# Kernel tuning notes

Measured on AMD Instinct MI355X. Metric: run time of the kernel, lower is better.

## Reference

```python
import jax, jax.numpy as jnp
import numpy as np

E, D, H, F = 3, 512, 8, 2048
B, V, L = 32, 21, 128
DH = D // H
EPS = 1e-5


def setup_inputs() -> dict:
    key = jax.random.key(0)
    ks = jax.random.split(key, 8)
    s = 0.02
    def p(k, shape):
        return (jax.random.normal(k, shape, jnp.float32) * s)
    return {
        "x": jax.random.normal(ks[0], (B, V, L, D), jnp.float32),
        "Wq": p(ks[1], (E, D, D)), "bq": jnp.zeros((E, D), jnp.float32),
        "Wk": p(ks[2], (E, D, D)), "bk": jnp.zeros((E, D), jnp.float32),
        "Wv": p(ks[3], (E, D, D)), "bv": jnp.zeros((E, D), jnp.float32),
        "Wo": p(ks[4], (E, D, D)), "bo": jnp.zeros((E, D), jnp.float32),
        "W1": p(ks[5], (E, D, F)), "b1": jnp.zeros((E, F), jnp.float32),
        "W2": p(ks[6], (E, F, D)), "b2": jnp.zeros((E, D), jnp.float32),
        "g1": jnp.ones((E, D), jnp.float32), "be1": jnp.zeros((E, D), jnp.float32),
        "g2": jnp.ones((E, D), jnp.float32), "be2": jnp.zeros((E, D), jnp.float32),
    }


def _batchnorm(x, gamma, beta):
    # x: [N, L, D]; BatchNorm1d(d_model) on x.transpose(-2,-1) == per-D-channel
    # stats over (N, L) axes (train-mode, biased variance).
    mean = jnp.mean(x, axis=(0, 1))
    var = jnp.var(x, axis=(0, 1))
    return (x - mean) * jax.lax.rsqrt(var + EPS) * gamma + beta


def _layer(x, prev_scores, Wq, bq, Wk, bk, Wv, bv, Wo, bo,
           W1, b1, W2, b2, g1, be1, g2, be2):
    N = x.shape[0]
    # multi-head projections -> [N, H, L, DH]
    q = (x @ Wq + bq).reshape(N, L, H, DH).transpose(0, 2, 1, 3)
    k = (x @ Wk + bk).reshape(N, L, H, DH).transpose(0, 2, 1, 3)
    v = (x @ Wv + bv).reshape(N, L, H, DH).transpose(0, 2, 1, 3)
    scores = jnp.einsum('nhld,nhmd->nhlm', q, k) / jnp.sqrt(jnp.float32(DH))
    if prev_scores is not None:
        scores = scores + prev_scores  # RealFormer-style residual score add
    attn = jax.nn.softmax(scores, axis=-1)
    ctx = jnp.einsum('nhlm,nhmd->nhld', attn, v)
    ctx = ctx.transpose(0, 2, 1, 3).reshape(N, L, D)
    x_ = ctx @ Wo + bo
    x = _batchnorm(x + x_, g1, be1)
    ffn = jax.nn.gelu(x @ W1 + b1, approximate=False) @ W2 + b2
    x = _batchnorm(x + ffn, g2, be2)
    return x, scores


def reference(x, Wq, bq, Wk, bk, Wv, bv, Wo, bo, W1, b1, W2, b2,
              g1, be1, g2, be2):
    h = x.reshape(-1, L, D)  # (B*V, L, D)
    scores = None
    for i in range(E):
        h, scores = _layer(h, scores,
                           Wq[i], bq[i], Wk[i], bk[i], Wv[i], bv[i],
                           Wo[i], bo[i], W1[i], b1[i], W2[i], b2[i],
                           g1[i], be1[i], g2[i], be2[i])
    return h
```

## Files before the change

kernel.cpp:

```cpp
#include <hip/hip_runtime.h>
#include <hip/hip_bf16.h>


typedef unsigned short u16;
typedef unsigned int u32;
typedef __attribute__((ext_vector_type(8))) short short8;
typedef __attribute__((ext_vector_type(4))) float floatx4;
typedef __attribute__((ext_vector_type(4))) unsigned short ushort4v;

#define DEV static __device__ __forceinline__

DEV u16 f2bf(float f) {
    union { float f; u32 u; } a; a.f = f;
    u32 r = a.u + 0x7FFF + ((a.u >> 16) & 1);
    return (u16)(r >> 16);
}
DEV float bf2f(u16 b) {
    union { u32 u; float f; } a; a.u = ((u32)b) << 16; return a.f;
}

DEV void gload16(const void* g, void* l) {
    __builtin_amdgcn_global_load_lds((const __attribute__((address_space(1))) void*)g,
                                     (__attribute__((address_space(3))) void*)l, 16, 0, 0);
}

__global__ void wtrans(const float* __restrict__ W, u16* __restrict__ out, int K, int N) {
    __shared__ float tile[32][33];
    const int k0 = blockIdx.x * 32, n0 = blockIdx.y * 32;
    const int tx = threadIdx.x & 31, ty = threadIdx.x >> 5;
#pragma unroll
    for (int j = 0; j < 4; ++j) {
        int r = ty + j * 8;
        tile[r][tx] = W[(size_t)(k0 + r) * N + n0 + tx];
    }
    __syncthreads();
#pragma unroll
    for (int j = 0; j < 4; ++j) {
        int r = ty + j * 8;
        out[(size_t)(n0 + r) * K + k0 + tx] = f2bf(tile[tx][r]);
    }
}

__global__ void bias_concat(const float* __restrict__ bq, const float* __restrict__ bk,
                            const float* __restrict__ bv, float* __restrict__ bqkv) {
    int t = blockIdx.x * 256 + threadIdx.x;
    if (t >= 3 * 1536) return;
    int e = t / 1536, c = t % 1536;
    float v = (c < 512) ? bq[e * 512 + c] : (c < 1024) ? bk[e * 512 + c - 512] : bv[e * 512 + c - 1024];
    bqkv[t] = v;
}

__global__ void xconvert(const float* __restrict__ x, u16* __restrict__ hb) {
    size_t i = ((size_t)blockIdx.x * 256 + threadIdx.x) * 8;
    float4 v0 = *(const float4*)&x[i];
    float4 v1 = *(const float4*)&x[i + 4];
    short8 o;
    o[0] = (short)f2bf(v0.x); o[1] = (short)f2bf(v0.y); o[2] = (short)f2bf(v0.z); o[3] = (short)f2bf(v0.w);
    o[4] = (short)f2bf(v1.x); o[5] = (short)f2bf(v1.y); o[6] = (short)f2bf(v1.z); o[7] = (short)f2bf(v1.w);
    *(short8*)&hb[i] = o;
}

template <int EPI>
__global__ __launch_bounds__(512)
void gemm_bt(const u16* __restrict__ A, int lda, const u16* __restrict__ Bt,
             const float* __restrict__ bias, const u16* __restrict__ res,
             u16* __restrict__ out, int N, int K, float* __restrict__ stats) {
    __shared__ u16 sA[2][4096];
    __shared__ u16 sB[2][4096];
    const int tid = threadIdx.x;
    const int wave = tid >> 6, lane = tid & 63;
    const int wm = wave >> 2, wn = wave & 3;
    const int m0 = blockIdx.y * 128, n0 = blockIdx.x * 128;
    const int fr = lane & 15, fq = lane >> 4;
    const int srow = lane >> 2, scol = (lane & 3) * 8;

    floatx4 acc[4][2] = {};
    const int NT = K >> 6;

    for (int kt = 0; kt < NT; ++kt) {
        __syncthreads();
        {
            const int ra = wave * 16 + srow;
            const size_t arow = (size_t)(m0 + ra) * lda + kt * 64 + scol;
            const size_t brow = (size_t)(n0 + ra) * (size_t)K + kt * 64 + scol;
#pragma unroll
            for (int kk = 0; kk < 2; ++kk) {
                gload16(A + arow + kk * 32, &sA[kk][wave * 512]);
                gload16(Bt + brow + kk * 32, &sB[kk][wave * 512]);
            }
        }
        __syncthreads();
#pragma unroll
        for (int kk = 0; kk < 2; ++kk) {
            short8 af[4], bfr[2];
#pragma unroll
            for (int m = 0; m < 4; ++m)
                af[m] = *(const short8*)&sA[kk][(wm * 64 + m * 16 + fr) * 32 + fq * 8];
#pragma unroll
            for (int nn = 0; nn < 2; ++nn)
                bfr[nn] = *(const short8*)&sB[kk][(wn * 32 + nn * 16 + fr) * 32 + fq * 8];
#pragma unroll
            for (int m = 0; m < 4; ++m)
#pragma unroll
                for (int nn = 0; nn < 2; ++nn)
                    acc[m][nn] = __builtin_amdgcn_mfma_f32_16x16x32_bf16(af[m], bfr[nn], acc[m][nn], 0, 0, 0);
        }
    }

    float ssum[2] = { 0.f, 0.f }, sqsum[2] = { 0.f, 0.f };
#pragma unroll
    for (int nn = 0; nn < 2; ++nn) {
        int col = n0 + wn * 32 + nn * 16 + fr;
        float bv = bias[col];
#pragma unroll
        for (int m = 0; m < 4; ++m) {
            int rowb = m0 + wm * 64 + m * 16 + fq * 4;
#pragma unroll
            for (int r = 0; r < 4; ++r) {
                size_t idx = (size_t)(rowb + r) * N + col;
                float v = acc[m][nn][r] + bv;
                if (EPI == 2) {
                    v += bf2f(res[idx]);
                    ssum[nn] += v;
                    sqsum[nn] += v * v;
                } else if (EPI == 1) {
                    v = 0.5f * v * (1.f + erff(v * 0.70710678118f));
                }
                out[idx] = f2bf(v);
            }
        }
    }
    if (EPI == 2) {
#pragma unroll
        for (int nn = 0; nn < 2; ++nn) {
            float s = ssum[nn], q = sqsum[nn];
            s += __shfl_xor(s, 16); s += __shfl_xor(s, 32);
            q += __shfl_xor(q, 16); q += __shfl_xor(q, 32);
            if (fq == 0) {
                int col = n0 + wn * 32 + nn * 16 + fr;
                atomicAdd(&stats[col], s);
                atomicAdd(&stats[512 + col], q);
            }
        }
    }
}

template <int HAS_PREV, int STORE_S>
__global__ __launch_bounds__(256)
void attn_kernel(u16* __restrict__ qkv, u16* __restrict__ scores) {
    const int bid = blockIdx.x;
    const int n = bid >> 3, h = bid & 7;
    const int tid = threadIdx.x, wave = tid >> 6, lane = tid & 63;
    const int wm = wave >> 1, wn = wave & 1;
    const int fr = lane & 15, fq = lane >> 4;

    __shared__ __align__(16) u16 uni[128 * 136];
    __shared__ __align__(16) u16 sV[64 * 136];
    __shared__ float sRed[128 * 2];

    u16 (*sQK)[128 * 32] = (u16(*)[128 * 32])uni;

    {
        const int t_ = wave;
        const int qk = t_ >> 1, kh = t_ & 1;
        const u16* base = qkv + (size_t)n * 128 * 1536 + qk * 512 + h * 64 + kh * 32 + (lane & 3) * 8;
        u16* dst = &sQK[t_][0];
        const int rr = lane >> 2;
#pragma unroll
        for (int c = 0; c < 8; ++c)
            gload16(base + (size_t)(c * 16 + rr) * 1536, dst + c * 512);
    }
    {
        const int mrow = tid >> 1;
        const int dh0 = (tid & 1) * 32;
        const u16* vsrc = qkv + (size_t)(n * 128 + mrow) * 1536 + 1024 + h * 64 + dh0;
#pragma unroll
        for (int j = 0; j < 4; ++j) {
            short8 vv = *(const short8*)&vsrc[j * 8];
#pragma unroll
            for (int e2 = 0; e2 < 8; ++e2)
                sV[(dh0 + j * 8 + e2) * 136 + mrow] = (u16)vv[e2];
        }
    }
    __syncthreads();

    floatx4 acc[4][4] = {};
#pragma unroll
    for (int kh = 0; kh < 2; ++kh) {
        short8 a[4], b[4];
#pragma unroll
        for (int m = 0; m < 4; ++m)
            a[m] = *(const short8*)&sQK[kh][(wm * 64 + m * 16 + fr) * 32 + fq * 8];
#pragma unroll
        for (int nn = 0; nn < 4; ++nn)
            b[nn] = *(const short8*)&sQK[2 + kh][(wn * 64 + nn * 16 + fr) * 32 + fq * 8];
#pragma unroll
        for (int m = 0; m < 4; ++m)
#pragma unroll
            for (int nn = 0; nn < 4; ++nn)
                acc[m][nn] = __builtin_amdgcn_mfma_f32_16x16x32_bf16(b[nn], a[m], acc[m][nn], 0, 0, 0);
    }

    const size_t tbase = ((size_t)bid * 256 + tid) * 64;
#pragma unroll
    for (int m = 0; m < 4; ++m) {
        short8 lo, hi;
        if (HAS_PREV) {
            lo = *(const short8*)&scores[tbase + m * 16];
            hi = *(const short8*)&scores[tbase + m * 16 + 8];
        }
#pragma unroll
        for (int nn = 0; nn < 4; ++nn)
#pragma unroll
            for (int r = 0; r < 4; ++r) {
                const int e = nn * 4 + r;
                float v = acc[m][nn][r] * 0.125f;
                if (HAS_PREV) v += bf2f((u16)(e < 8 ? lo[e] : hi[e - 8]));
                acc[m][nn][r] = v;
            }
        if (STORE_S) {
            short8 slo, shi;
#pragma unroll
            for (int nn = 0; nn < 4; ++nn)
#pragma unroll
                for (int r = 0; r < 4; ++r) {
                    const int e = nn * 4 + r;
                    u16 bv = f2bf(acc[m][nn][r]);
                    if (e < 8) slo[e] = (short)bv; else shi[e - 8] = (short)bv;
                }
            *(short8*)&scores[tbase + m * 16] = slo;
            *(short8*)&scores[tbase + m * 16 + 8] = shi;
        }
    }

#pragma unroll
    for (int m = 0; m < 4; ++m) {
        const int row = wm * 64 + m * 16 + fr;
        float mx = acc[m][0][0];
#pragma unroll
        for (int nn = 0; nn < 4; ++nn)
#pragma unroll
            for (int r = 0; r < 4; ++r) mx = fmaxf(mx, acc[m][nn][r]);
        mx = fmaxf(mx, __shfl_xor(mx, 16));
        mx = fmaxf(mx, __shfl_xor(mx, 32));
        if (fq == 0) sRed[row * 2 + wn] = mx;
    }
    __syncthreads();

    float rmax[4];
#pragma unroll
    for (int m = 0; m < 4; ++m) {
        const int row = wm * 64 + m * 16 + fr;
        rmax[m] = fmaxf(sRed[row * 2], sRed[row * 2 + 1]);
    }
    __syncthreads();

    u16* sP = uni;
#pragma unroll
    for (int m = 0; m < 4; ++m) {
        const int row = wm * 64 + m * 16 + fr;
        float sm = 0.f;
#pragma unroll
        for (int nn = 0; nn < 4; ++nn) {
#pragma unroll
            for (int r = 0; r < 4; ++r) {
                float p = __expf(acc[m][nn][r] - rmax[m]);
                acc[m][nn][r] = p;
                sm += p;
            }
        }
        sm += __shfl_xor(sm, 16);
        sm += __shfl_xor(sm, 32);
        if (fq == 0) sRed[row * 2 + wn] = sm;
#pragma unroll
        for (int nn = 0; nn < 4; ++nn) {
            ushort4v pv = { f2bf(acc[m][nn][0]), f2bf(acc[m][nn][1]),
                            f2bf(acc[m][nn][2]), f2bf(acc[m][nn][3]) };
            *(ushort4v*)&sP[row * 136 + wn * 64 + nn * 16 + fq * 4] = pv;
        }
    }
    __syncthreads();

    floatx4 acc2[4][2] = {};
#pragma unroll
    for (int k0 = 0; k0 < 128; k0 += 32) {
        short8 a[4], b[2];
#pragma unroll
        for (int m = 0; m < 4; ++m)
            a[m] = *(const short8*)&sP[(wm * 64 + m * 16 + fr) * 136 + k0 + fq * 8];
#pragma unroll
        for (int n2 = 0; n2 < 2; ++n2)
            b[n2] = *(const short8*)&sV[(wn * 32 + n2 * 16 + fr) * 136 + k0 + fq * 8];
#pragma unroll
        for (int m = 0; m < 4; ++m)
#pragma unroll
            for (int n2 = 0; n2 < 2; ++n2)
                acc2[m][n2] = __builtin_amdgcn_mfma_f32_16x16x32_bf16(b[n2], a[m], acc2[m][n2], 0, 0, 0);
    }

#pragma unroll
    for (int m = 0; m < 4; ++m) {
        const int row = wm * 64 + m * 16 + fr;
        const float inv = 1.f / (sRed[row * 2] + sRed[row * 2 + 1]);
#pragma unroll
        for (int n2 = 0; n2 < 2; ++n2) {
            const int dhb = wn * 32 + n2 * 16 + fq * 4;
            ushort4v o = { f2bf(acc2[m][n2][0] * inv), f2bf(acc2[m][n2][1] * inv),
                           f2bf(acc2[m][n2][2] * inv), f2bf(acc2[m][n2][3] * inv) };
            *(ushort4v*)&qkv[(size_t)(n * 128 + row) * 1536 + h * 64 + dhb] = o;
        }
    }
}

__global__ void zero_stats(float* s) { s[threadIdx.x] = 0.f; }

__global__ void bn_finalize(float* stats, int M) {
    int c = blockIdx.x * 256 + threadIdx.x;
    if (c >= 512) return;
    float mean = stats[c] / M;
    float var = stats[512 + c] / M - mean * mean;
    stats[c] = mean;
    stats[512 + c] = rsqrtf(var + 1e-5f);
}

template <int FINAL>
__global__ void bn_apply(const u16* __restrict__ y, const float* __restrict__ stats,
                         const float* __restrict__ gamma, const float* __restrict__ beta,
                         u16* __restrict__ outb, float* __restrict__ outf) {
    size_t i = ((size_t)blockIdx.x * 256 + threadIdx.x) * 8;
    short8 v = *(const short8*)&y[i];
    int c = (int)(i & 511);
    float o[8];
#pragma unroll
    for (int j = 0; j < 8; ++j) {
        float f = bf2f((u16)v[j]);
        o[j] = (f - stats[c + j]) * stats[512 + c + j] * gamma[c + j] + beta[c + j];
    }
    if (FINAL) {
        float4 a = { o[0], o[1], o[2], o[3] }, b = { o[4], o[5], o[6], o[7] };
        *(float4*)&outf[i] = a;
        *(float4*)&outf[i + 4] = b;
    } else {
        short8 ob;
#pragma unroll
        for (int j = 0; j < 8; ++j) ob[j] = (short)f2bf(o[j]);
        *(short8*)&outb[i] = ob;
    }
}

extern "C" void kernel_launch(void* const* d_in, const int* in_sizes, int n_in,
                              void* d_out, int out_size, void* d_ws, size_t ws_size,
                              hipStream_t stream) {
    const float* x  = (const float*)d_in[0];
    const float* Wq = (const float*)d_in[1];  const float* bq = (const float*)d_in[2];
    const float* Wk = (const float*)d_in[3];  const float* bk = (const float*)d_in[4];
    const float* Wv = (const float*)d_in[5];  const float* bv = (const float*)d_in[6];
    const float* Wo = (const float*)d_in[7];  const float* bo = (const float*)d_in[8];
    const float* W1 = (const float*)d_in[9];  const float* b1 = (const float*)d_in[10];
    const float* W2 = (const float*)d_in[11]; const float* b2 = (const float*)d_in[12];
    const float* g1 = (const float*)d_in[13]; const float* be1 = (const float*)d_in[14];
    const float* g2 = (const float*)d_in[15]; const float* be2 = (const float*)d_in[16];

    const int M = 86016;
    const int MC = 43008;

    char* ws = (char*)d_ws;
    size_t off = 0;
    auto alloc = [&](size_t bytes) -> void* {
        void* p = ws + off;
        off = (off + bytes + 255) & ~(size_t)255;
        return p;
    };
    u16* scores = (u16*)alloc((size_t)5376 * 16384 * 2);
    u16* hb     = (u16*)alloc((size_t)M * 512 * 2);
    u16* qkv    = (u16*)alloc((size_t)M * 1536 * 2);
    u16* Wqkvt  = (u16*)alloc((size_t)3 * 1536 * 512 * 2);
    u16* Wot    = (u16*)alloc((size_t)3 * 512 * 512 * 2);
    u16* W1t    = (u16*)alloc((size_t)3 * 2048 * 512 * 2);
    u16* W2t    = (u16*)alloc((size_t)3 * 512 * 2048 * 2);
    float* bqkv = (float*)alloc((size_t)3 * 1536 * 4);
    float* stats = (float*)alloc(1024 * 4);

    if (off > ws_size) return;

    for (int e = 0; e < 3; ++e) {
        wtrans<<<dim3(16, 16), 256, 0, stream>>>(Wq + (size_t)e * 512 * 512, Wqkvt + (size_t)e * 1536 * 512, 512, 512);
        wtrans<<<dim3(16, 16), 256, 0, stream>>>(Wk + (size_t)e * 512 * 512, Wqkvt + (size_t)e * 1536 * 512 + 512 * 512, 512, 512);
        wtrans<<<dim3(16, 16), 256, 0, stream>>>(Wv + (size_t)e * 512 * 512, Wqkvt + (size_t)e * 1536 * 512 + 1024 * 512, 512, 512);
        wtrans<<<dim3(16, 16), 256, 0, stream>>>(Wo + (size_t)e * 512 * 512, Wot + (size_t)e * 512 * 512, 512, 512);
        wtrans<<<dim3(16, 64), 256, 0, stream>>>(W1 + (size_t)e * 512 * 2048, W1t + (size_t)e * 2048 * 512, 512, 2048);
        wtrans<<<dim3(64, 16), 256, 0, stream>>>(W2 + (size_t)e * 2048 * 512, W2t + (size_t)e * 512 * 2048, 2048, 512);
    }
    bias_concat<<<18, 256, 0, stream>>>(bq, bk, bv, bqkv);
    xconvert<<<21504, 256, 0, stream>>>(x, hb);

    for (int e = 0; e < 3; ++e) {
        gemm_bt<0><<<dim3(12, 672), 512, 0, stream>>>(hb, 512, Wqkvt + (size_t)e * 1536 * 512,
                                                      bqkv + e * 1536, nullptr, qkv, 1536, 512, nullptr);
        if (e == 0)      attn_kernel<0, 1><<<5376, 256, 0, stream>>>(qkv, scores);
        else if (e == 1) attn_kernel<1, 1><<<5376, 256, 0, stream>>>(qkv, scores);
        else             attn_kernel<1, 0><<<5376, 256, 0, stream>>>(qkv, scores);
        zero_stats<<<1, 1024, 0, stream>>>(stats);
        gemm_bt<2><<<dim3(4, 672), 512, 0, stream>>>(qkv, 1536, Wot + (size_t)e * 512 * 512,
                                                     bo + e * 512, hb, hb, 512, 512, stats);
        bn_finalize<<<2, 256, 0, stream>>>(stats, M);
        bn_apply<0><<<21504, 256, 0, stream>>>(hb, stats, g1 + e * 512, be1 + e * 512, hb, nullptr);
        zero_stats<<<1, 1024, 0, stream>>>(stats);
        for (int c = 0; c < 2; ++c) {
            const u16* hc = hb + (size_t)c * MC * 512;
            gemm_bt<1><<<dim3(16, 336), 512, 0, stream>>>(hc, 512, W1t + (size_t)e * 2048 * 512,
                                                          b1 + e * 2048, nullptr, qkv, 2048, 512, nullptr);
            gemm_bt<2><<<dim3(4, 336), 512, 0, stream>>>(qkv, 2048, W2t + (size_t)e * 512 * 2048,
                                                         b2 + e * 512, hc, (u16*)hc, 512, 2048, stats);
        }
        bn_finalize<<<2, 256, 0, stream>>>(stats, M);
        if (e < 2)
            bn_apply<0><<<21504, 256, 0, stream>>>(hb, stats, g2 + e * 512, be2 + e * 512, hb, nullptr);
        else
            bn_apply<1><<<21504, 256, 0, stream>>>(hb, stats, g2 + e * 512, be2 + e * 512, nullptr, (float*)d_out);
    }
    (void)in_sizes; (void)n_in; (void)out_size;
}
```

Before: 3.273 ms.

## Fold BatchNorm affine into next-layer weights, biases and residual epilogue

Drops the separate BatchNorm apply passes over the activation buffer. The per-channel scale is folded into the transposed bf16 weights of the following GEMM (QKV or W1), and the shift is folded into its bias through a small matvec. The residual GEMM epilogue (new EPI 3) applies the same scale and shift to the un-normalized residual on the fly, so only the final output still needs an apply pass. Weight transposes are also batched over experts with a z grid dimension. Rescaling bf16 weights in place adds a second rounding step, and the normalized activation is never stored explicitly.

```diff
diff --git a/kernel.cpp b/kernel.cpp
--- a/kernel.cpp
+++ b/kernel.cpp
@@ -24,7 +24,10 @@
                                      (__attribute__((address_space(3))) void*)l, 16, 0, 0);
 }
 
-__global__ void wtrans(const float* __restrict__ W, u16* __restrict__ out, int K, int N) {
+__global__ void wtrans(const float* __restrict__ W, u16* __restrict__ out, int K, int N,
+                       int inStride, int outStride) {
+    W += (size_t)blockIdx.z * inStride;
+    out += (size_t)blockIdx.z * outStride;
     __shared__ float tile[32][33];
     const int k0 = blockIdx.x * 32, n0 = blockIdx.y * 32;
     const int tx = threadIdx.x & 31, ty = threadIdx.x >> 5;
@@ -60,11 +63,51 @@
     *(short8*)&hb[i] = o;
 }
 
+__global__ void zero_stats2(float* raw) { raw[blockIdx.x * 1024 + threadIdx.x] = 0.f; }
+
+__global__ void bn_finalize_st(const float* __restrict__ raw, const float* __restrict__ g,
+                               const float* __restrict__ be, float* __restrict__ fin, int M) {
+    int c = blockIdx.x * 256 + threadIdx.x;
+    if (c >= 512) return;
+    float mean = raw[c] / M;
+    float var = raw[512 + c] / M - mean * mean;
+    float s = rsqrtf(var + 1e-5f) * g[c];
+    fin[512 + c] = s;
+    fin[c] = be[c] - mean * s;
+}
+
+__global__ void bias_fold(const u16* __restrict__ Wt, const float* __restrict__ bias_in,
+                          const float* __restrict__ fin, float* __restrict__ bias_out) {
+    __shared__ float tsh[512];
+    for (int i = threadIdx.x; i < 512; i += 256) tsh[i] = fin[i];
+    __syncthreads();
+    int n = blockIdx.x * 256 + threadIdx.x;
+    const u16* w = Wt + (size_t)n * 512;
+    float acc = bias_in[n];
+    for (int k = 0; k < 512; k += 8) {
+        short8 wv = *(const short8*)&w[k];
+#pragma unroll
+        for (int j = 0; j < 8; ++j) acc += tsh[k + j] * bf2f((u16)wv[j]);
+    }
+    bias_out[n] = acc;
+}
+
+__global__ void weight_scale(u16* __restrict__ Wt, const float* __restrict__ fin) {
+    size_t i = ((size_t)blockIdx.x * 256 + threadIdx.x) * 8;
+    int k = (int)(i & 511);
+    short8 w = *(short8*)&Wt[i];
+    short8 o;
+#pragma unroll
+    for (int j = 0; j < 8; ++j) o[j] = (short)f2bf(bf2f((u16)w[j]) * fin[512 + k + j]);
+    *(short8*)&Wt[i] = o;
+}
+
 template <int EPI>
 __global__ __launch_bounds__(512)
 void gemm_bt(const u16* __restrict__ A, int lda, const u16* __restrict__ Bt,
              const float* __restrict__ bias, const u16* __restrict__ res,
-             u16* __restrict__ out, int N, int K, float* __restrict__ stats) {
+             u16* __restrict__ out, int N, int K, float* __restrict__ stats,
+             const float* __restrict__ finRes) {
     __shared__ u16 sA[2][4096];
     __shared__ u16 sB[2][4096];
     const int tid = threadIdx.x;
@@ -112,6 +155,8 @@
     for (int nn = 0; nn < 2; ++nn) {
         int col = n0 + wn * 32 + nn * 16 + fr;
         float bv = bias[col];
+        float rs = 0.f, rt = 0.f;
+        if (EPI == 3) { rs = finRes[512 + col]; rt = finRes[col]; }
 #pragma unroll
         for (int m = 0; m < 4; ++m) {
             int rowb = m0 + wm * 64 + m * 16 + fq * 4;
@@ -121,8 +166,10 @@
                 float v = acc[m][nn][r] + bv;
                 if (EPI == 2) {
                     v += bf2f(res[idx]);
-                    ssum[nn] += v;
-                    sqsum[nn] += v * v;
+                    ssum[nn] += v; sqsum[nn] += v * v;
+                } else if (EPI == 3) {
+                    v += rs * bf2f(res[idx]) + rt;
+                    ssum[nn] += v; sqsum[nn] += v * v;
                 } else if (EPI == 1) {
                     v = 0.5f * v * (1.f + erff(v * 0.70710678118f));
                 }
@@ -130,7 +177,7 @@
             }
         }
     }
-    if (EPI == 2) {
+    if (EPI == 2 || EPI == 3) {
 #pragma unroll
         for (int nn = 0; nn < 2; ++nn) {
             float s = ssum[nn], q = sqsum[nn];
@@ -312,40 +359,18 @@
     }
 }
 
-__global__ void zero_stats(float* s) { s[threadIdx.x] = 0.f; }
-
-__global__ void bn_finalize(float* stats, int M) {
-    int c = blockIdx.x * 256 + threadIdx.x;
-    if (c >= 512) return;
-    float mean = stats[c] / M;
-    float var = stats[512 + c] / M - mean * mean;
-    stats[c] = mean;
-    stats[512 + c] = rsqrtf(var + 1e-5f);
-}
-
-template <int FINAL>
-__global__ void bn_apply(const u16* __restrict__ y, const float* __restrict__ stats,
-                         const float* __restrict__ gamma, const float* __restrict__ beta,
-                         u16* __restrict__ outb, float* __restrict__ outf) {
+__global__ void bn_apply_final(const u16* __restrict__ y, const float* __restrict__ fin,
+                               float* __restrict__ outf) {
     size_t i = ((size_t)blockIdx.x * 256 + threadIdx.x) * 8;
     short8 v = *(const short8*)&y[i];
     int c = (int)(i & 511);
     float o[8];
 #pragma unroll
-    for (int j = 0; j < 8; ++j) {
-        float f = bf2f((u16)v[j]);
-        o[j] = (f - stats[c + j]) * stats[512 + c + j] * gamma[c + j] + beta[c + j];
-    }
-    if (FINAL) {
-        float4 a = { o[0], o[1], o[2], o[3] }, b = { o[4], o[5], o[6], o[7] };
-        *(float4*)&outf[i] = a;
-        *(float4*)&outf[i + 4] = b;
-    } else {
-        short8 ob;
-#pragma unroll
-        for (int j = 0; j < 8; ++j) ob[j] = (short)f2bf(o[j]);
-        *(short8*)&outb[i] = ob;
-    }
+    for (int j = 0; j < 8; ++j)
+        o[j] = bf2f((u16)v[j]) * fin[512 + c + j] + fin[c + j];
+    float4 a = { o[0], o[1], o[2], o[3] }, b = { o[4], o[5], o[6], o[7] };
+    *(float4*)&outf[i] = a;
+    *(float4*)&outf[i + 4] = b;
 }
 
 extern "C" void kernel_launch(void* const* d_in, const int* in_sizes, int n_in,
@@ -379,45 +404,57 @@
     u16* W1t    = (u16*)alloc((size_t)3 * 2048 * 512 * 2);
     u16* W2t    = (u16*)alloc((size_t)3 * 512 * 2048 * 2);
     float* bqkv = (float*)alloc((size_t)3 * 1536 * 4);
-    float* stats = (float*)alloc(1024 * 4);
+    float* raw  = (float*)alloc(2048 * 4);
+    float* fin1 = (float*)alloc(1024 * 4);
+    float* fin2 = (float*)alloc(1024 * 4);
+    float* biasQ = (float*)alloc(1536 * 4);
+    float* biasF = (float*)alloc(2048 * 4);
+    float* raw1 = raw, *raw2 = raw + 1024;
 
     if (off > ws_size) return;
 
-    for (int e = 0; e < 3; ++e) {
-        wtrans<<<dim3(16, 16), 256, 0, stream>>>(Wq + (size_t)e * 512 * 512, Wqkvt + (size_t)e * 1536 * 512, 512, 512);
-        wtrans<<<dim3(16, 16), 256, 0, stream>>>(Wk + (size_t)e * 512 * 512, Wqkvt + (size_t)e * 1536 * 512 + 512 * 512, 512, 512);
-        wtrans<<<dim3(16, 16), 256, 0, stream>>>(Wv + (size_t)e * 512 * 512, Wqkvt + (size_t)e * 1536 * 512 + 1024 * 512, 512, 512);
-        wtrans<<<dim3(16, 16), 256, 0, stream>>>(Wo + (size_t)e * 512 * 512, Wot + (size_t)e * 512 * 512, 512, 512);
-        wtrans<<<dim3(16, 64), 256, 0, stream>>>(W1 + (size_t)e * 512 * 2048, W1t + (size_t)e * 2048 * 512, 512, 2048);
-        wtrans<<<dim3(64, 16), 256, 0, stream>>>(W2 + (size_t)e * 2048 * 512, W2t + (size_t)e * 512 * 2048, 2048, 512);
-    }
+    wtrans<<<dim3(16, 16, 3), 256, 0, stream>>>(Wq, Wqkvt,                 512, 512,  512 * 512, 1536 * 512);
+    wtrans<<<dim3(16, 16, 3), 256, 0, stream>>>(Wk, Wqkvt + 512 * 512,     512, 512,  512 * 512, 1536 * 512);
+    wtrans<<<dim3(16, 16, 3), 256, 0, stream>>>(Wv, Wqkvt + 1024 * 512,    512, 512,  512 * 512, 1536 * 512);
+    wtrans<<<dim3(16, 16, 3), 256, 0, stream>>>(Wo, Wot,                   512, 512,  512 * 512, 512 * 512);
+    wtrans<<<dim3(16, 64, 3), 256, 0, stream>>>(W1, W1t,                   512, 2048, 512 * 2048, 2048 * 512);
+    wtrans<<<dim3(64, 16, 3), 256, 0, stream>>>(W2, W2t,                   2048, 512, 2048 * 512, 512 * 2048);
     bias_concat<<<18, 256, 0, stream>>>(bq, bk, bv, bqkv);
     xconvert<<<21504, 256, 0, stream>>>(x, hb);
 
     for (int e = 0; e < 3; ++e) {
-        gemm_bt<0><<<dim3(12, 672), 512, 0, stream>>>(hb, 512, Wqkvt + (size_t)e * 1536 * 512,
-                                                      bqkv + e * 1536, nullptr, qkv, 1536, 512, nullptr);
+        u16* Wqkv_e = Wqkvt + (size_t)e * 1536 * 512;
+        u16* W1_e   = W1t + (size_t)e * 2048 * 512;
+        if (e > 0) {
+            bias_fold<<<6, 256, 0, stream>>>(Wqkv_e, bqkv + e * 1536, fin2, biasQ);
+            weight_scale<<<384, 256, 0, stream>>>(Wqkv_e, fin2);
+        }
+        gemm_bt<0><<<dim3(12, 672), 512, 0, stream>>>(hb, 512, Wqkv_e,
+                                                      e ? biasQ : bqkv + e * 1536,
+                                                      nullptr, qkv, 1536, 512, nullptr, nullptr);
         if (e == 0)      attn_kernel<0, 1><<<5376, 256, 0, stream>>>(qkv, scores);
         else if (e == 1) attn_kernel<1, 1><<<5376, 256, 0, stream>>>(qkv, scores);
         else             attn_kernel<1, 0><<<5376, 256, 0, stream>>>(qkv, scores);
-        zero_stats<<<1, 1024, 0, stream>>>(stats);
-        gemm_bt<2><<<dim3(4, 672), 512, 0, stream>>>(qkv, 1536, Wot + (size_t)e * 512 * 512,
-                                                     bo + e * 512, hb, hb, 512, 512, stats);
-        bn_finalize<<<2, 256, 0, stream>>>(stats, M);
-        bn_apply<0><<<21504, 256, 0, stream>>>(hb, stats, g1 + e * 512, be1 + e * 512, hb, nullptr);
-        zero_stats<<<1, 1024, 0, stream>>>(stats);
+        zero_stats2<<<2, 1024, 0, stream>>>(raw);
+        if (e == 0)
+            gemm_bt<2><<<dim3(4, 672), 512, 0, stream>>>(qkv, 1536, Wot + (size_t)e * 512 * 512,
+                                                         bo + e * 512, hb, hb, 512, 512, raw1, nullptr);
+        else
+            gemm_bt<3><<<dim3(4, 672), 512, 0, stream>>>(qkv, 1536, Wot + (size_t)e * 512 * 512,
+                                                         bo + e * 512, hb, hb, 512, 512, raw1, fin2);
+        bn_finalize_st<<<2, 256, 0, stream>>>(raw1, g1 + e * 512, be1 + e * 512, fin1, M);
+        bias_fold<<<8, 256, 0, stream>>>(W1_e, b1 + e * 2048, fin1, biasF);
+        weight_scale<<<512, 256, 0, stream>>>(W1_e, fin1);
         for (int c = 0; c < 2; ++c) {
             const u16* hc = hb + (size_t)c * MC * 512;
-            gemm_bt<1><<<dim3(16, 336), 512, 0, stream>>>(hc, 512, W1t + (size_t)e * 2048 * 512,
-                                                          b1 + e * 2048, nullptr, qkv, 2048, 512, nullptr);
-            gemm_bt<2><<<dim3(4, 336), 512, 0, stream>>>(qkv, 2048, W2t + (size_t)e * 512 * 2048,
-                                                         b2 + e * 512, hc, (u16*)hc, 512, 2048, stats);
-        }
-        bn_finalize<<<2, 256, 0, stream>>>(stats, M);
-        if (e < 2)
-            bn_apply<0><<<21504, 256, 0, stream>>>(hb, stats, g2 + e * 512, be2 + e * 512, hb, nullptr);
-        else
-            bn_apply<1><<<21504, 256, 0, stream>>>(hb, stats, g2 + e * 512, be2 + e * 512, nullptr, (float*)d_out);
+            gemm_bt<1><<<dim3(16, 336), 512, 0, stream>>>(hc, 512, W1_e,
+                                                          biasF, nullptr, qkv, 2048, 512, nullptr, nullptr);
+            gemm_bt<3><<<dim3(4, 336), 512, 0, stream>>>(qkv, 2048, W2t + (size_t)e * 512 * 2048,
+                                                         b2 + e * 512, hc, (u16*)hc, 512, 2048, raw2, fin1);
+        }
+        bn_finalize_st<<<2, 256, 0, stream>>>(raw2, g2 + e * 512, be2 + e * 512, fin2, M);
+        if (e == 2)
+            bn_apply_final<<<21504, 256, 0, stream>>>(hb, fin2, (float*)d_out);
     }
     (void)in_sizes; (void)n_in; (void)out_size;
 }
```

Result: slower. 3.706 ms (+13.2%).
